# Kernel tuning notes

Measured on AMD Instinct MI355X. Metric: run time of the kernel, lower is better.

Reference implementation:

```python
import jax, jax.numpy as jnp
import numpy as np

MAX_DISPARITY = 192


def _cost_volume(L, R, D):
    """Banded stereo correlation.

    cost[n, j, h, x] = sum_c L[n,c,h,x] * R[n,c,h,x-j], zero when x < j.
    Equivalent to the original full (W,W) matmul followed by per-disparity
    diagonal extraction + left zero-pad, but computed as D shifted
    dot-products (honors the banded structure).
    """
    N, C, H, W = L.shape
    Rp = jnp.pad(R, ((0, 0), (0, 0), (0, 0), (D - 1, 0)))  # left zero-pad

    def step(_, j):
        Rs = jax.lax.dynamic_slice_in_dim(Rp, D - 1 - j, W, axis=3)  # R shifted right by j
        c = jnp.einsum('nchw,nchw->nhw', L, Rs)
        return None, c

    _, cv = jax.lax.scan(step, None, jnp.arange(D))  # (D, N, H, W)
    return jnp.transpose(cv, (1, 0, 2, 3))  # (N, D, H, W)


def setup_inputs() -> dict:
    key = jax.random.key(0)
    ks = jax.random.split(key, 6)
    shapes = [(1, 32, 256, 512), (1, 32, 128, 256), (1, 32, 64, 128)]
    inp = {}
    for i, s in enumerate(shapes):
        inp[f'left{i}'] = jax.random.normal(ks[2 * i], s, dtype=jnp.float32)
        inp[f'right{i}'] = jax.random.normal(ks[2 * i + 1], s, dtype=jnp.float32)
    return inp


def reference(left0, right0, left1, right1, left2, right2):
    lefts = [left0, left1, left2]
    rights = [right0, right1, right2]
    max_disparity = min(MAX_DISPARITY, lefts[0].shape[-1])
    cost_volumes = []
    for i, (L, R) in enumerate(zip(lefts, rights)):
        D = max_disparity // (2 ** i)
        cost_volumes.append(_cost_volume(L, R, D))
    return tuple(cost_volumes)
```

## Files before the change

kernel.cpp:

```cpp
#include <hip/hip_runtime.h>


#define NBLK_TOTAL 1344
#define SRB 80
#define EPT 272
#define EPW 1088

typedef float vf4 __attribute__((ext_vector_type(4)));
typedef float f32x4 __attribute__((ext_vector_type(4)));
typedef _Float16 h4 __attribute__((ext_vector_type(4)));
typedef _Float16 h8 __attribute__((ext_vector_type(8)));

template<int DG>
__device__ __forceinline__ void epilogue_w(const f32x4 (&acc0)[13], const f32x4 (&acc1)[13],
                                           float* __restrict__ Ew, float* __restrict__ o,
                                           int H, int W, int h, int xw,
                                           int l, int lm, int kg)
{
    const int jo0 = l >> 3;
    const int xbl = (l & 7) * 4;
    const int mt  = xbl >> 4;
    const int mb  = xbl & 15;
    const int dep = lm * 17 + 4 * kg;

    #pragma unroll
    for (int jg = 0; jg < DG; ++jg) {
        if (jg == 0) {
            *(f32x4*)&Ew[(0 * 2 + 0) * EPT + dep] = acc0[12];
            *(f32x4*)&Ew[(1 * 2 + 0) * EPT + dep] = acc1[12];
        }
        {
            const int slot = (11 - jg) & 1;
            *(f32x4*)&Ew[(0 * 2 + slot) * EPT + dep] = acc0[11 - jg];
            *(f32x4*)&Ew[(1 * 2 + slot) * EPT + dep] = acc1[11 - jg];
        }
        const int s12 = jg & 1;
        const int s11 = s12 ^ 1;
        #pragma unroll
        for (int r = 0; r < 2; ++r) {
            int jo = 8 * r + jo0;
            int j  = 16 * jg + jo;
            vf4 v;
            #pragma unroll
            for (int i = 0; i < 4; ++i) {
                int m = mb + i;
                int slot = (m >= jo) ? s12 : s11;
                int n = (m - jo) & 15;
                v[i] = Ew[(mt * 2 + slot) * EPT + n * 17 + m];
            }
            float* p = o + ((size_t)j * H + h) * W + xw + xbl;
            __builtin_nontemporal_store(v, (vf4*)p);
        }
    }
}

__global__ __launch_bounds__(256, 3)
void cost_volume_fused(const float* __restrict__ L0, const float* __restrict__ R0,
                       const float* __restrict__ L1, const float* __restrict__ R1,
                       const float* __restrict__ L2, const float* __restrict__ R2,
                       float* __restrict__ out)
{
    __shared__ __align__(16) char St[448 * SRB];
    __shared__ __align__(16) float Ep[4 * EPW];

    const int id = (blockIdx.x & 7) * 168 + (blockIdx.x >> 3);

    const float* L; const float* R; float* o;
    int H, W, D, bx, h;
    if (id < 1024) {
        L = L0; R = R0; o = out;
        H = 256; W = 512; D = 192;
        bx = id & 3; h = id >> 2;
    } else if (id < 1280) {
        int r = id - 1024;
        L = L1; R = R1; o = out + (size_t)192 * 256 * 512;
        H = 128; W = 256; D = 96;
        bx = r & 1; h = r >> 1;
    } else {
        int r = id - 1280;
        L = L2; R = R2; o = out + (size_t)192 * 256 * 512 + (size_t)96 * 128 * 256;
        H = 64; W = 128; D = 48;
        bx = 0; h = r;
    }

    const int x0 = bx * 128;
    const int t  = threadIdx.x;
    const int l  = t & 63;
    const int w_ = t >> 6;

    const size_t HW = (size_t)H * W;
    const float* Lb = L + (size_t)h * W;
    const float* Rb = R + (size_t)h * W;

    char* Sb = (char*)St;

    {
        const int c0 = (t >> 5) * 4;
        const int x4 = t & 31;
        const float* gp = Lb + (size_t)c0 * HW + x0 + 4 * x4;
        vf4 v0 = *(const vf4*)(gp);
        vf4 v1 = *(const vf4*)(gp + HW);
        vf4 v2 = *(const vf4*)(gp + 2 * HW);
        vf4 v3 = *(const vf4*)(gp + 3 * HW);
        const int chk = (((c0 >> 3) ^ (x4 & 3)) << 4) | ((c0 & 7) << 1);
        #pragma unroll
        for (int xi = 0; xi < 4; ++xi) {
            int row = 4 * x4 + xi;
            h4 hv = { (_Float16)v0[xi], (_Float16)v1[xi],
                      (_Float16)v2[xi], (_Float16)v3[xi] };
            *(h4*)(Sb + row * SRB + chk) = hv;
        }
    }
    #pragma unroll
    for (int k = 0; k < 3; ++k) {
        int idm = t + k * 256;
        if (idm < 640) {
            int c0 = (idm / 80) * 4;
            int x4 = idm - (idm / 80) * 80;
            int g = x0 - 192 + 4 * x4;
            vf4 v0 = (vf4)(0.f), v1 = (vf4)(0.f), v2 = (vf4)(0.f), v3 = (vf4)(0.f);
            if (g >= 0) {
                const float* gp = Rb + (size_t)c0 * HW + g;
                v0 = *(const vf4*)(gp);
                v1 = *(const vf4*)(gp + HW);
                v2 = *(const vf4*)(gp + 2 * HW);
                v3 = *(const vf4*)(gp + 3 * HW);
            }
            const int chk = (((c0 >> 3) ^ (x4 & 3)) << 4) | ((c0 & 7) << 1);
            #pragma unroll
            for (int xi = 0; xi < 4; ++xi) {
                int row = 128 + 4 * x4 + xi;
                h4 hv = { (_Float16)v0[xi], (_Float16)v1[xi],
                          (_Float16)v2[xi], (_Float16)v3[xi] };
                *(h4*)(Sb + row * SRB + chk) = hv;
            }
        }
    }
    __syncthreads();

    const int lm = l & 15;
    const int kg = l >> 4;
    const int q0 = 2 * w_;
    const int rsw = (lm >> 2) & 3;

    f32x4 acc0[13], acc1[13];
    #pragma unroll
    for (int i = 0; i < 13; ++i) { acc0[i] = (f32x4)(0.f); acc1[i] = (f32x4)(0.f); }

    const int rowA0 = 16 * q0 + lm;
    const int rowA1 = rowA0 + 16;
    h8 a0 = *(const h8*)(Sb + rowA0 * SRB + ((kg ^ rsw) << 4));
    h8 a1 = *(const h8*)(Sb + rowA1 * SRB + ((kg ^ rsw) << 4));

    #pragma unroll
    for (int nt = 0; nt <= 13; ++nt) {
        int rowB = 128 + 16 * (q0 + nt) + lm;
        h8 b = *(const h8*)(Sb + rowB * SRB + ((kg ^ rsw) << 4));
        if (nt <= 12)
            acc0[nt] = __builtin_amdgcn_mfma_f32_16x16x32_f16(a0, b, acc0[nt], 0, 0, 0);
        if (nt >= 1)
            acc1[nt - 1] = __builtin_amdgcn_mfma_f32_16x16x32_f16(a1, b, acc1[nt - 1], 0, 0, 0);
    }

    float* Ew = Ep + w_ * EPW;
    const int xw = x0 + 32 * w_;
    if (D == 192)      epilogue_w<12>(acc0, acc1, Ew, o, H, W, h, xw, l, lm, kg);
    else if (D == 96)  epilogue_w<6>(acc0, acc1, Ew, o, H, W, h, xw, l, lm, kg);
    else               epilogue_w<3>(acc0, acc1, Ew, o, H, W, h, xw, l, lm, kg);
}

extern "C" void kernel_launch(void* const* d_in, const int* in_sizes, int n_in,
                              void* d_out, int out_size, void* d_ws, size_t ws_size,
                              hipStream_t stream)
{
    const float* L0 = (const float*)d_in[0];
    const float* R0 = (const float*)d_in[1];
    const float* L1 = (const float*)d_in[2];
    const float* R1 = (const float*)d_in[3];
    const float* L2 = (const float*)d_in[4];
    const float* R2 = (const float*)d_in[5];
    float* out = (float*)d_out;

    cost_volume_fused<<<dim3(NBLK_TOTAL), dim3(256), 0, stream>>>(
        L0, R0, L1, R1, L2, R2, out);
}
```

Before: 167.5 us.

## Split level-0 disparity range across two blocks and alias epilogue LDS

Level-0 work is split so each block handles 96 disparities instead of 192, which doubles the block count and halves the accumulator arrays per thread. The epilogue scratch now reuses the staging LDS after a barrier, which removes the separate epilogue buffer. Launch bounds are raised to 4 blocks per CU to increase occupancy. In exchange, the L tile is loaded and converted twice for level-0 rows, an extra __syncthreads is added, and the grid has more blocks to schedule.

```diff
diff --git a/kernel.cpp b/kernel.cpp
--- a/kernel.cpp
+++ b/kernel.cpp
@@ -1,8 +1,9 @@
 #include <hip/hip_runtime.h>
 
 
-#define NBLK_TOTAL 1344
+#define NBLK_TOTAL 2368
 #define SRB 80
+#define NRW 352
 #define EPT 272
 #define EPW 1088
 
@@ -12,9 +13,9 @@
 typedef _Float16 h8 __attribute__((ext_vector_type(8)));
 
 template<int DG>
-__device__ __forceinline__ void epilogue_w(const f32x4 (&acc0)[13], const f32x4 (&acc1)[13],
+__device__ __forceinline__ void epilogue_w(const f32x4 (&acc0)[7], const f32x4 (&acc1)[7],
                                            float* __restrict__ Ew, float* __restrict__ o,
-                                           int H, int W, int h, int xw,
+                                           int H, int W, int h, int j0, int xw,
                                            int l, int lm, int kg)
 {
     const int jo0 = l >> 3;
@@ -26,25 +27,25 @@
     #pragma unroll
     for (int jg = 0; jg < DG; ++jg) {
         if (jg == 0) {
-            *(f32x4*)&Ew[(0 * 2 + 0) * EPT + dep] = acc0[12];
-            *(f32x4*)&Ew[(1 * 2 + 0) * EPT + dep] = acc1[12];
+            *(f32x4*)&Ew[(0 * 2 + 0) * EPT + dep] = acc0[6];
+            *(f32x4*)&Ew[(1 * 2 + 0) * EPT + dep] = acc1[6];
         }
         {
-            const int slot = (11 - jg) & 1;
-            *(f32x4*)&Ew[(0 * 2 + slot) * EPT + dep] = acc0[11 - jg];
-            *(f32x4*)&Ew[(1 * 2 + slot) * EPT + dep] = acc1[11 - jg];
+            const int slot = (5 - jg) & 1;
+            *(f32x4*)&Ew[(0 * 2 + slot) * EPT + dep] = acc0[5 - jg];
+            *(f32x4*)&Ew[(1 * 2 + slot) * EPT + dep] = acc1[5 - jg];
         }
-        const int s12 = jg & 1;
-        const int s11 = s12 ^ 1;
+        const int s6 = jg & 1;
+        const int s5 = s6 ^ 1;
         #pragma unroll
         for (int r = 0; r < 2; ++r) {
             int jo = 8 * r + jo0;
-            int j  = 16 * jg + jo;
+            int j  = j0 + 16 * jg + jo;
             vf4 v;
             #pragma unroll
             for (int i = 0; i < 4; ++i) {
                 int m = mb + i;
-                int slot = (m >= jo) ? s12 : s11;
+                int slot = (m >= jo) ? s6 : s5;
                 int n = (m - jo) & 15;
                 v[i] = Ew[(mt * 2 + slot) * EPT + n * 17 + m];
             }
@@ -54,36 +55,36 @@
     }
 }
 
-__global__ __launch_bounds__(256, 3)
+__global__ __launch_bounds__(256, 4)
 void cost_volume_fused(const float* __restrict__ L0, const float* __restrict__ R0,
                        const float* __restrict__ L1, const float* __restrict__ R1,
                        const float* __restrict__ L2, const float* __restrict__ R2,
                        float* __restrict__ out)
 {
-    __shared__ __align__(16) char St[448 * SRB];
-    __shared__ __align__(16) float Ep[4 * EPW];
+    __shared__ __align__(16) char St[NRW * SRB];
 
-    const int id = (blockIdx.x & 7) * 168 + (blockIdx.x >> 3);
+    const int id = (blockIdx.x & 7) * 296 + (blockIdx.x >> 3);
 
     const float* L; const float* R; float* o;
-    int H, W, D, bx, h;
-    if (id < 1024) {
+    int H, W, D, bx, h, j0, DG;
+    if (id < 2048) {
         L = L0; R = R0; o = out;
         H = 256; W = 512; D = 192;
-        bx = id & 3; h = id >> 2;
-    } else if (id < 1280) {
-        int r = id - 1024;
+        j0 = (id & 1) * 96; bx = (id >> 1) & 3; h = id >> 3; DG = 6;
+    } else if (id < 2304) {
+        int r = id - 2048;
         L = L1; R = R1; o = out + (size_t)192 * 256 * 512;
         H = 128; W = 256; D = 96;
-        bx = r & 1; h = r >> 1;
+        j0 = 0; bx = r & 1; h = r >> 1; DG = 6;
     } else {
-        int r = id - 1280;
+        int r = id - 2304;
         L = L2; R = R2; o = out + (size_t)192 * 256 * 512 + (size_t)96 * 128 * 256;
         H = 64; W = 128; D = 48;
-        bx = 0; h = r;
+        j0 = 0; bx = 0; h = r; DG = 3;
     }
 
     const int x0 = bx * 128;
+    const int GB = x0 - j0 - 96;
     const int t  = threadIdx.x;
     const int l  = t & 63;
     const int w_ = t >> 6;
@@ -112,12 +113,12 @@
         }
     }
     #pragma unroll
-    for (int k = 0; k < 3; ++k) {
+    for (int k = 0; k < 2; ++k) {
         int idm = t + k * 256;
-        if (idm < 640) {
-            int c0 = (idm / 80) * 4;
-            int x4 = idm - (idm / 80) * 80;
-            int g = x0 - 192 + 4 * x4;
+        if (idm < 448) {
+            int c0 = (idm / 56) * 4;
+            int x4 = idm - (idm / 56) * 56;
+            int g = GB + 4 * x4;
             vf4 v0 = (vf4)(0.f), v1 = (vf4)(0.f), v2 = (vf4)(0.f), v3 = (vf4)(0.f);
             if (g >= 0) {
                 const float* gp = Rb + (size_t)c0 * HW + g;
@@ -143,9 +144,9 @@
     const int q0 = 2 * w_;
     const int rsw = (lm >> 2) & 3;
 
-    f32x4 acc0[13], acc1[13];
+    f32x4 acc0[7], acc1[7];
     #pragma unroll
-    for (int i = 0; i < 13; ++i) { acc0[i] = (f32x4)(0.f); acc1[i] = (f32x4)(0.f); }
+    for (int i = 0; i < 7; ++i) { acc0[i] = (f32x4)(0.f); acc1[i] = (f32x4)(0.f); }
 
     const int rowA0 = 16 * q0 + lm;
     const int rowA1 = rowA0 + 16;
@@ -153,20 +154,21 @@
     h8 a1 = *(const h8*)(Sb + rowA1 * SRB + ((kg ^ rsw) << 4));
 
     #pragma unroll
-    for (int nt = 0; nt <= 13; ++nt) {
+    for (int nt = 0; nt <= 7; ++nt) {
         int rowB = 128 + 16 * (q0 + nt) + lm;
         h8 b = *(const h8*)(Sb + rowB * SRB + ((kg ^ rsw) << 4));
-        if (nt <= 12)
+        if (nt <= 6)
             acc0[nt] = __builtin_amdgcn_mfma_f32_16x16x32_f16(a0, b, acc0[nt], 0, 0, 0);
         if (nt >= 1)
             acc1[nt - 1] = __builtin_amdgcn_mfma_f32_16x16x32_f16(a1, b, acc1[nt - 1], 0, 0, 0);
     }
 
-    float* Ew = Ep + w_ * EPW;
+    __syncthreads();
+
+    float* Ew = (float*)St + w_ * EPW;
     const int xw = x0 + 32 * w_;
-    if (D == 192)      epilogue_w<12>(acc0, acc1, Ew, o, H, W, h, xw, l, lm, kg);
-    else if (D == 96)  epilogue_w<6>(acc0, acc1, Ew, o, H, W, h, xw, l, lm, kg);
-    else               epilogue_w<3>(acc0, acc1, Ew, o, H, W, h, xw, l, lm, kg);
+    if (DG == 6) epilogue_w<6>(acc0, acc1, Ew, o, H, W, h, j0, xw, l, lm, kg);
+    else         epilogue_w<3>(acc0, acc1, Ew, o, H, W, h, j0, xw, l, lm, kg);
 }
 
 extern "C" void kernel_launch(void* const* d_in, const int* in_sizes, int n_in,
```

Result: faster. 163.3 us (-2.6%).
